# Kernel optimization log

Measured on AMD Instinct MI355X. Metric: run time of the kernel, lower is better.

The kernel has to match this reference:

```python
import jax, jax.numpy as jnp
import numpy as np

EPS = 1e-5  # BatchNorm1d default eps
HEADS = 4


def _batchnorm(x, gamma, beta):
    # BatchNorm1d applied per graph: stats over node axis (axis=1), biased var (training mode)
    mean = x.mean(axis=1, keepdims=True)
    var = x.var(axis=1, keepdims=True)
    return gamma * (x - mean) * jax.lax.rsqrt(var + EPS) + beta


def setup_inputs() -> dict:
    key = jax.random.key(0)
    ks = jax.random.split(key, 8)
    B, N, F_in, C = 4, 4096, 128, 64
    inputs = jax.random.normal(ks[0], (B, N, F_in), jnp.float32)
    # sparse-ish adjacency (avg degree ~16); only used for non-emptiness check since conv=None
    adj = (jax.random.uniform(ks[1], (B, N, N)) < 0.004).astype(jnp.float32)
    s = lambda k, shp, fan: jax.random.normal(k, shp, jnp.float32) / np.sqrt(fan)
    return dict(
        inputs=inputs, adj=adj,
        Wp=s(ks[2], (C, F_in), F_in), bp=jnp.zeros((C,), jnp.float32),      # project Linear
        Wqkv=s(ks[3], (3 * C, C), C), bqkv=jnp.zeros((3 * C,), jnp.float32),  # MHA in_proj
        Wo=s(ks[4], (C, C), C), bo=jnp.zeros((C,), jnp.float32),            # MHA out_proj
        g2=jnp.ones((C,), jnp.float32), b2=jnp.zeros((C,), jnp.float32),    # norm2 (BatchNorm)
        W1=s(ks[5], (2 * C, C), C), b1=jnp.zeros((2 * C,), jnp.float32),    # MLP Linear 1
        W2=s(ks[6], (C, 2 * C), 2 * C), b2m=jnp.zeros((C,), jnp.float32),   # MLP Linear 2
        g3=jnp.ones((C,), jnp.float32), b3=jnp.zeros((C,), jnp.float32),    # norm3 (BatchNorm)
    )


def reference(inputs, adj, Wp, bp, Wqkv, bqkv, Wo, bo, g2, b2, W1, b1, W2, b2m, g3, b3):
    B, N, _ = inputs.shape
    C = Wp.shape[0]
    Dh = C // HEADS
    # project in_features -> out_features
    x = jnp.einsum('bnf,cf->bnc', inputs, Wp) + bp
    # GPSConv with conv=None: only the global multi-head self-attention branch runs
    qkv = jnp.einsum('bnc,dc->bnd', x, Wqkv) + bqkv
    q, k, v = jnp.split(qkv, 3, axis=-1)
    rs = lambda t: t.reshape(B, N, HEADS, Dh)
    q, k, v = rs(q), rs(k), rs(v)
    scores = jnp.einsum('bnhd,bmhd->bhnm', q, k) / np.sqrt(Dh).astype(np.float32)
    attn = jax.nn.softmax(scores, axis=-1)
    o = jnp.einsum('bhnm,bmhd->bnhd', attn, v).reshape(B, N, C)
    h = jnp.einsum('bnc,oc->bno', o, Wo) + bo
    # residual + norm2
    h = _batchnorm(h + x, g2, b2)
    # out = h (sum of single-branch hs); out = out + mlp(out); norm3
    mlp = jnp.einsum('bnk,ck->bnc',
                     jax.nn.relu(jnp.einsum('bnc,kc->bnk', h, W1) + b1),
                     W2) + b2m
    out = _batchnorm(h + mlp, g3, b3)
    # wrapper applies tanh (edge_index non-empty)
    return jnp.tanh(out)
```

## Files before the change

kernel.cpp:

```cpp
#include <hip/hip_runtime.h>
#include <hip/hip_bf16.h>

constexpr int NN = 4096;
constexpr int CC = 64;
constexpr int NH = 4;
constexpr int DH = 16;
constexpr int KSPLIT = 4;

typedef _Float16 f16x4 __attribute__((ext_vector_type(4)));
typedef float f32x4 __attribute__((ext_vector_type(4)));

#define QSCALE 0.36067376022224085f
#define L2E2   2.8853900817779268f

#if defined(__has_builtin)
#if __has_builtin(__builtin_amdgcn_exp2f)
#define FAST_EXP2(x) __builtin_amdgcn_exp2f(x)
#endif
#if __has_builtin(__builtin_amdgcn_rcpf)
#define FAST_RCP(x) __builtin_amdgcn_rcpf(x)
#endif
#endif
#ifndef FAST_EXP2
#define FAST_EXP2(x) exp2f(x)
#endif
#ifndef FAST_RCP
#define FAST_RCP(x) (1.0f / (x))
#endif

__device__ __forceinline__ float fast_tanh(float x) {
  const float t = FAST_EXP2(x * L2E2);
  return fmaf(-2.f, FAST_RCP(t + 1.f), 1.f);
}

__global__ __launch_bounds__(256) void proj_qkv_k(
    const float* __restrict__ inp, const float* __restrict__ Wp,
    const float* __restrict__ bp, const float* __restrict__ Wqkv,
    const float* __restrict__ bqkv, float* __restrict__ xout,
    _Float16* __restrict__ f16b)
{
  __shared__ __align__(16) float As[64][68];
  __shared__ __align__(16) float Xs[64][68];
  __shared__ __align__(16) float W2s[64][196];

  const int tid = threadIdx.x;
  const int rowbase = blockIdx.x * 64;
  const int r4 = (tid & 15) * 4;
  const int cg = (tid >> 4) * 4;
  const int cg2 = (tid >> 4) * 12;

  float acc[4][4];
  #pragma unroll
  for (int i = 0; i < 4; ++i)
    #pragma unroll
    for (int j = 0; j < 4; ++j) acc[i][j] = 0.f;

  for (int k0 = 0; k0 < 128; k0 += 64) {
    if (k0) __syncthreads();
    #pragma unroll
    for (int i = 0; i < 16; ++i) {
      int idx = tid + i * 256;
      int c2 = idx >> 6, kk = idx & 63;
      Xs[kk][c2] = Wp[(size_t)c2 * 128 + k0 + kk];
    }
    #pragma unroll
    for (int i = 0; i < 16; ++i) {
      int idx = tid + i * 256;
      int r = idx >> 6, kk = idx & 63;
      As[kk][r] = inp[(size_t)(rowbase + r) * 128 + k0 + kk];
    }
    __syncthreads();
    #pragma unroll 4
    for (int kk = 0; kk < 64; ++kk) {
      const float4 a = *(const float4*)&As[kk][r4];
      const float4 w4 = *(const float4*)&Xs[kk][cg];
      const float av[4] = {a.x, a.y, a.z, a.w};
      const float wv[4] = {w4.x, w4.y, w4.z, w4.w};
      #pragma unroll
      for (int ri = 0; ri < 4; ++ri)
        #pragma unroll
        for (int ci = 0; ci < 4; ++ci)
          acc[ri][ci] = fmaf(av[ri], wv[ci], acc[ri][ci]);
    }
  }

  float xv[4][4];
  #pragma unroll
  for (int ri = 0; ri < 4; ++ri)
    #pragma unroll
    for (int j = 0; j < 4; ++j) {
      xv[ri][j] = acc[ri][j] + bp[cg + j];
      xout[(size_t)(rowbase + r4 + ri) * CC + cg + j] = xv[ri][j];
    }

  __syncthreads();
  #pragma unroll
  for (int ri = 0; ri < 4; ++ri)
    #pragma unroll
    for (int j = 0; j < 4; ++j)
      Xs[cg + j][r4 + ri] = xv[ri][j];
  #pragma unroll
  for (int i = 0; i < 48; ++i) {
    int idx = tid + i * 256;
    int c2 = idx >> 6, kk = idx & 63;
    W2s[kk][c2] = Wqkv[(size_t)c2 * 64 + kk];
  }
  __syncthreads();

  float acc2[4][12];
  #pragma unroll
  for (int i = 0; i < 4; ++i)
    #pragma unroll
    for (int j = 0; j < 12; ++j) acc2[i][j] = 0.f;

  #pragma unroll 4
  for (int kk = 0; kk < 64; ++kk) {
    const float4 a = *(const float4*)&Xs[kk][r4];
    const float av[4] = {a.x, a.y, a.z, a.w};
    #pragma unroll
    for (int cj = 0; cj < 3; ++cj) {
      const float4 w4 = *(const float4*)&W2s[kk][cg2 + cj * 4];
      const float wv[4] = {w4.x, w4.y, w4.z, w4.w};
      #pragma unroll
      for (int ri = 0; ri < 4; ++ri)
        #pragma unroll
        for (int ci = 0; ci < 4; ++ci)
          acc2[ri][cj * 4 + ci] = fmaf(av[ri], wv[ci], acc2[ri][cj * 4 + ci]);
    }
  }

  #pragma unroll
  for (int ri = 0; ri < 4; ++ri) {
    const int row = rowbase + r4 + ri;
    const int n = row & (NN - 1);
    const int bq = (row >> 12) * NH;
    #pragma unroll
    for (int j = 0; j < 12; ++j) {
      float v = acc2[ri][j] + bqkv[cg2 + j];
      const int c2 = cg2 + j;
      const int which = c2 >> 6;
      const int hc = c2 & 63;
      const int bh = bq + (hc >> 4);
      const int d = hc & 15;
      if (which == 0) v *= QSCALE;
      if (which < 2)
        f16b[(size_t)which * 1048576 + ((size_t)bh * NN + n) * DH + d] = (_Float16)v;
      else
        f16b[2097152 + ((size_t)bh * DH + d) * NN + n] = (_Float16)v;
    }
  }
}

__global__ __launch_bounds__(256, 6) void attn_k(
    const _Float16* __restrict__ qb, const _Float16* __restrict__ kb,
    const _Float16* __restrict__ vtb, float* __restrict__ po,
    float* __restrict__ rs)
{
  __shared__ _Float16 Kl[64][20];
  __shared__ _Float16 Vl[16][72];

  const int bid = blockIdx.x;
  const int xcd = bid & 7;
  const int rest = bid >> 3;
  const int bh = 2 * xcd + (rest & 1);
  const int ks = (rest >> 1) & 3;
  const int n0 = (rest >> 3) * 128;
  const int tid = threadIdx.x;
  const int w = tid >> 6;
  const int l = tid & 63;
  const int g = l >> 4, i = l & 15;
  const int qbase = n0 + w * 32;
  const int kbeg = ks * (NN / KSPLIT);

  const _Float16* __restrict__ qhp = qb + (size_t)bh * NN * DH;
  const _Float16* __restrict__ khp = kb + (size_t)bh * NN * DH;
  const _Float16* __restrict__ vhp = vtb + (size_t)bh * DH * NN;

  const f16x4 qfA = *(const f16x4*)(qhp + (size_t)(qbase + i) * DH + 4 * g);
  const f16x4 qfB = *(const f16x4*)(qhp + (size_t)(qbase + 16 + i) * DH + 4 * g);

  f32x4 oA = {0.f, 0.f, 0.f, 0.f}, oB = {0.f, 0.f, 0.f, 0.f};
  const f32x4 zz = {0.f, 0.f, 0.f, 0.f};
  float rsA = 0.f, rsB = 0.f;

  const int srow = tid >> 2, spart = (tid & 3) * 4;
  const int sd = tid >> 4, scol = (tid & 15) * 4;

  f16x4 kr = *(const f16x4*)(khp + (size_t)(kbeg + srow) * DH + spart);
  f16x4 vr = *(const f16x4*)(vhp + (size_t)sd * NN + kbeg + scol);

  constexpr int NCH = (NN / KSPLIT) / 64;
  for (int c = 0; c < NCH; ++c) {
    *(f16x4*)&Kl[srow][spart] = kr;
    *(f16x4*)&Vl[sd][scol] = vr;
    __syncthreads();
    if (c + 1 < NCH) {
      const int nx = kbeg + (c + 1) * 64;
      kr = *(const f16x4*)(khp + (size_t)(nx + srow) * DH + spart);
      vr = *(const f16x4*)(vhp + (size_t)sd * NN + nx + scol);
    }

    #pragma unroll
    for (int kk = 0; kk < 64; kk += 16) {
      const f16x4 kf = *(const f16x4*)&Kl[kk + i][4 * g];
      const f16x4 vf = *(const f16x4*)&Vl[i][kk + 4 * g];
      f32x4 sA = __builtin_amdgcn_mfma_f32_16x16x16f16(kf, qfA, zz, 0, 0, 0);
      f32x4 sB = __builtin_amdgcn_mfma_f32_16x16x16f16(kf, qfB, zz, 0, 0, 0);
      const float a0 = FAST_EXP2(sA[0]), a1 = FAST_EXP2(sA[1]),
                  a2 = FAST_EXP2(sA[2]), a3 = FAST_EXP2(sA[3]);
      const float b0 = FAST_EXP2(sB[0]), b1 = FAST_EXP2(sB[1]),
                  b2 = FAST_EXP2(sB[2]), b3 = FAST_EXP2(sB[3]);
      rsA += (a0 + a1) + (a2 + a3);
      rsB += (b0 + b1) + (b2 + b3);
      const auto alo = __builtin_amdgcn_cvt_pkrtz(a0, a1);
      const auto ahi = __builtin_amdgcn_cvt_pkrtz(a2, a3);
      const auto blo = __builtin_amdgcn_cvt_pkrtz(b0, b1);
      const auto bhi = __builtin_amdgcn_cvt_pkrtz(b2, b3);
      f16x4 pA, pB;
      pA[0] = (_Float16)alo[0]; pA[1] = (_Float16)alo[1];
      pA[2] = (_Float16)ahi[0]; pA[3] = (_Float16)ahi[1];
      pB[0] = (_Float16)blo[0]; pB[1] = (_Float16)blo[1];
      pB[2] = (_Float16)bhi[0]; pB[3] = (_Float16)bhi[1];
      oA = __builtin_amdgcn_mfma_f32_16x16x16f16(pA, vf, oA, 0, 0, 0);
      oB = __builtin_amdgcn_mfma_f32_16x16x16f16(pB, vf, oB, 0, 0, 0);
    }
    __syncthreads();
  }

  rsA += __shfl_xor(rsA, 16); rsA += __shfl_xor(rsA, 32);
  rsB += __shfl_xor(rsB, 16); rsB += __shfl_xor(rsB, 32);

  float* __restrict__ pob = po + (size_t)(ks * 16 + bh) * NN * DH;
  #pragma unroll
  for (int r = 0; r < 4; ++r) {
    const int ql = 4 * g + r;
    pob[(size_t)(qbase + ql) * DH + i] = oA[r];
    pob[(size_t)(qbase + 16 + ql) * DH + i] = oB[r];
  }
  if (g == 0) {
    float* __restrict__ rsb = rs + (size_t)(ks * 16 + bh) * NN;
    rsb[qbase + i] = rsA;
    rsb[qbase + 16 + i] = rsB;
  }
}

__global__ __launch_bounds__(256) void wo_red_k(
    const float* __restrict__ po, const float* __restrict__ rs,
    const float* __restrict__ Wo, const float* __restrict__ bo,
    const float* __restrict__ xin, float* __restrict__ out)
{
  __shared__ __align__(16) float As[64][68];
  __shared__ __align__(16) float Ws[64][68];
  __shared__ float Linv[64][4];

  const int tid = threadIdx.x;
  const int rowbase = blockIdx.x * 64;
  const int r4 = (tid & 15) * 4;
  const int cg = (tid >> 4) * 4;

  {
    const int r = tid & 63, hb = tid >> 6;
    const int row = rowbase + r;
    const int bh = (row >> 12) * NH + hb;
    const int n = row & (NN - 1);
    const float s = rs[(size_t)bh * NN + n] + rs[(size_t)(16 + bh) * NN + n] +
                    rs[(size_t)(32 + bh) * NN + n] + rs[(size_t)(48 + bh) * NN + n];
    Linv[r][hb] = 1.f / s;
  }
  #pragma unroll
  for (int i = 0; i < 16; ++i) {
    int idx = tid + i * 256;
    int c2 = idx >> 6, kk = idx & 63;
    Ws[kk][c2] = Wo[(size_t)c2 * 64 + kk];
  }
  __syncthreads();
  #pragma unroll
  for (int i = 0; i < 16; ++i) {
    int idx = tid + i * 256;
    int r = idx >> 6, kk = idx & 63;
    const int row = rowbase + r;
    const int bh = (row >> 12) * NH + (kk >> 4);
    const int n = row & (NN - 1);
    const int d = kk & 15;
    const size_t base = (((size_t)bh * NN + n) * DH) + d;
    const float v = po[base] + po[base + 1048576] +
                    po[base + 2097152] + po[base + 3145728];
    As[kk][r] = v * Linv[r][kk >> 4];
  }
  __syncthreads();

  float acc[4][4];
  #pragma unroll
  for (int i = 0; i < 4; ++i)
    #pragma unroll
    for (int j = 0; j < 4; ++j) acc[i][j] = 0.f;

  #pragma unroll 4
  for (int kk = 0; kk < 64; ++kk) {
    const float4 a = *(const float4*)&As[kk][r4];
    const float4 w4 = *(const float4*)&Ws[kk][cg];
    const float av[4] = {a.x, a.y, a.z, a.w};
    const float wv[4] = {w4.x, w4.y, w4.z, w4.w};
    #pragma unroll
    for (int ri = 0; ri < 4; ++ri)
      #pragma unroll
      for (int ci = 0; ci < 4; ++ci)
        acc[ri][ci] = fmaf(av[ri], wv[ci], acc[ri][ci]);
  }

  #pragma unroll
  for (int ri = 0; ri < 4; ++ri) {
    const int row = rowbase + r4 + ri;
    #pragma unroll
    for (int j = 0; j < 4; ++j) {
      const int c = cg + j;
      out[(size_t)row * CC + c] =
          acc[ri][j] + bo[c] + xin[(size_t)row * CC + c];
    }
  }
}

__global__ __launch_bounds__(256) void mlp_k(
    const float* __restrict__ hf, const float* __restrict__ W1,
    const float* __restrict__ b1, const float* __restrict__ W2,
    const float* __restrict__ b2m, float* __restrict__ out)
{
  __shared__ __align__(16) float As[64][68];
  __shared__ __align__(16) float Wbuf[8704];
  __shared__ __align__(16) float Ts[128][68];

  const int tid = threadIdx.x;
  const int rowbase = blockIdx.x * 64;
  const int r4 = (tid & 15) * 4;
  const int cg8 = (tid >> 4) * 8;
  const int cg4 = (tid >> 4) * 4;

  #pragma unroll
  for (int i = 0; i < 32; ++i) {
    int idx = tid + i * 256;
    int c2 = idx >> 6, kk = idx & 63;
    Wbuf[kk * 132 + c2] = W1[(size_t)c2 * 64 + kk];
  }
  #pragma unroll
  for (int i = 0; i < 16; ++i) {
    int idx = tid + i * 256;
    int r = idx >> 6, kk = idx & 63;
    As[kk][r] = hf[(size_t)(rowbase + r) * CC + kk];
  }
  __syncthreads();

  float acc1[4][8];
  #pragma unroll
  for (int i = 0; i < 4; ++i)
    #pragma unroll
    for (int j = 0; j < 8; ++j) acc1[i][j] = 0.f;

  #pragma unroll 4
  for (int kk = 0; kk < 64; ++kk) {
    const float4 a = *(const float4*)&As[kk][r4];
    const float av[4] = {a.x, a.y, a.z, a.w};
    #pragma unroll
    for (int cj = 0; cj < 2; ++cj) {
      const float4 w4 = *(const float4*)&Wbuf[kk * 132 + cg8 + cj * 4];
      const float wv[4] = {w4.x, w4.y, w4.z, w4.w};
      #pragma unroll
      for (int ri = 0; ri < 4; ++ri)
        #pragma unroll
        for (int ci = 0; ci < 4; ++ci)
          acc1[ri][cj * 4 + ci] = fmaf(av[ri], wv[ci], acc1[ri][cj * 4 + ci]);
    }
  }
  #pragma unroll
  for (int ri = 0; ri < 4; ++ri)
    #pragma unroll
    for (int j = 0; j < 8; ++j)
      Ts[cg8 + j][r4 + ri] = fmaxf(acc1[ri][j] + b1[cg8 + j], 0.f);
  __syncthreads();

  #pragma unroll
  for (int i = 0; i < 32; ++i) {
    int idx = tid + i * 256;
    int c2 = idx >> 7, kk = idx & 127;
    Wbuf[kk * 68 + c2] = W2[(size_t)c2 * 128 + kk];
  }
  __syncthreads();

  float acc2[4][4];
  #pragma unroll
  for (int i = 0; i < 4; ++i)
    #pragma unroll
    for (int j = 0; j < 4; ++j) acc2[i][j] = 0.f;

  #pragma unroll 4
  for (int kk = 0; kk < 128; ++kk) {
    const float4 a = *(const float4*)&Ts[kk][r4];
    const float4 w4 = *(const float4*)&Wbuf[kk * 68 + cg4];
    const float av[4] = {a.x, a.y, a.z, a.w};
    const float wv[4] = {w4.x, w4.y, w4.z, w4.w};
    #pragma unroll
    for (int ri = 0; ri < 4; ++ri)
      #pragma unroll
      for (int ci = 0; ci < 4; ++ci)
        acc2[ri][ci] = fmaf(av[ri], wv[ci], acc2[ri][ci]);
  }

  #pragma unroll
  for (int ri = 0; ri < 4; ++ri) {
    const int row = rowbase + r4 + ri;
    #pragma unroll
    for (int j = 0; j < 4; ++j) {
      const int c = cg4 + j;
      out[(size_t)row * CC + c] = acc2[ri][j] + b2m[c] + As[c][r4 + ri];
    }
  }
}

__global__ __launch_bounds__(256) void bn4_k(
    const float* __restrict__ in, const float* __restrict__ g,
    const float* __restrict__ b, float* __restrict__ out, int do_tanh)
{
  const int bb = blockIdx.x >> 4;
  const int c4 = (blockIdx.x & 15) * 4;
  const float* __restrict__ base = in + (size_t)bb * NN * CC + c4;
  const int tid = threadIdx.x;

  float4 s = {0, 0, 0, 0}, sq = {0, 0, 0, 0};
  #pragma unroll
  for (int i = 0; i < 16; ++i) {
    const float4 v = *(const float4*)&base[(size_t)(tid + i * 256) * CC];
    s.x += v.x; s.y += v.y; s.z += v.z; s.w += v.w;
    sq.x = fmaf(v.x, v.x, sq.x); sq.y = fmaf(v.y, v.y, sq.y);
    sq.z = fmaf(v.z, v.z, sq.z); sq.w = fmaf(v.w, v.w, sq.w);
  }
  #pragma unroll
  for (int off = 32; off; off >>= 1) {
    s.x += __shfl_down(s.x, off); s.y += __shfl_down(s.y, off);
    s.z += __shfl_down(s.z, off); s.w += __shfl_down(s.w, off);
    sq.x += __shfl_down(sq.x, off); sq.y += __shfl_down(sq.y, off);
    sq.z += __shfl_down(sq.z, off); sq.w += __shfl_down(sq.w, off);
  }
  __shared__ float red[4][8];
  const int wv = tid >> 6;
  if ((tid & 63) == 0) {
    red[wv][0] = s.x; red[wv][1] = s.y; red[wv][2] = s.z; red[wv][3] = s.w;
    red[wv][4] = sq.x; red[wv][5] = sq.y; red[wv][6] = sq.z; red[wv][7] = sq.w;
  }
  __syncthreads();
  float scale[4], shift[4];
  #pragma unroll
  for (int j = 0; j < 4; ++j) {
    const float ts = red[0][j] + red[1][j] + red[2][j] + red[3][j];
    const float tq = red[0][4 + j] + red[1][4 + j] + red[2][4 + j] + red[3][4 + j];
    const float mean = ts * (1.f / NN);
    const float var = tq * (1.f / NN) - mean * mean;
    const float rstd = rsqrtf(var + 1e-5f);
    scale[j] = g[c4 + j] * rstd;
    shift[j] = b[c4 + j] - mean * scale[j];
  }
  float* __restrict__ ob = out + (size_t)bb * NN * CC + c4;
  #pragma unroll
  for (int i = 0; i < 16; ++i) {
    const size_t idx = (size_t)(tid + i * 256) * CC;
    const float4 v = *(const float4*)&base[idx];
    float4 o;
    o.x = v.x * scale[0] + shift[0];
    o.y = v.y * scale[1] + shift[1];
    o.z = v.z * scale[2] + shift[2];
    o.w = v.w * scale[3] + shift[3];
    if (do_tanh) {
      o.x = fast_tanh(o.x); o.y = fast_tanh(o.y);
      o.z = fast_tanh(o.z); o.w = fast_tanh(o.w);
    }
    *(float4*)&ob[idx] = o;
  }
}

extern "C" void kernel_launch(void* const* d_in, const int* in_sizes, int n_in,
                              void* d_out, int out_size, void* d_ws, size_t ws_size,
                              hipStream_t stream)
{
  const float* inp  = (const float*)d_in[0];
  const float* Wp   = (const float*)d_in[2];
  const float* bp   = (const float*)d_in[3];
  const float* Wqkv = (const float*)d_in[4];
  const float* bqkv = (const float*)d_in[5];
  const float* Wo   = (const float*)d_in[6];
  const float* bo   = (const float*)d_in[7];
  const float* g2   = (const float*)d_in[8];
  const float* b2   = (const float*)d_in[9];
  const float* W1   = (const float*)d_in[10];
  const float* b1   = (const float*)d_in[11];
  const float* W2   = (const float*)d_in[12];
  const float* b2m  = (const float*)d_in[13];
  const float* g3   = (const float*)d_in[14];
  const float* b3   = (const float*)d_in[15];

  float* w = (float*)d_ws;
  float* x    = w;
  float* qkvA = w + 1048576;
  float* hf   = w + 2621440;
  float* pf   = w + 3670016;
  float* poW  = w + 4718592;
  float* rsW  = w + 8912896;

  _Float16* f16b = (_Float16*)qkvA;

  proj_qkv_k<<<dim3(256), dim3(256), 0, stream>>>(inp, Wp, bp, Wqkv, bqkv, x, f16b);
  attn_k<<<dim3(2048), dim3(256), 0, stream>>>(f16b, f16b + 1048576,
                                               f16b + 2097152, poW, rsW);
  wo_red_k<<<dim3(256), dim3(256), 0, stream>>>(poW, rsW, Wo, bo, x, hf);
  bn4_k<<<dim3(64), dim3(256), 0, stream>>>(hf, g2, b2, hf, 0);
  mlp_k<<<dim3(256), dim3(256), 0, stream>>>(hf, W1, b1, W2, b2m, pf);
  bn4_k<<<dim3(64), dim3(256), 0, stream>>>(pf, g3, b3, (float*)d_out, 1);
}
```

Baseline: 125.7 us.

## Split fused projection+QKV kernel into four templated GEMM launches

Replaces the single fused input-projection and QKV kernel with a generic templated GEMM that runs as four launches: the projection, then separate Q, K and V^T GEMMs reading x back from global memory. This likely aims at lower register and LDS use per launch, and so higher occupancy, than the 48-accumulator fused kernel. In exchange it adds three kernel launches and re-reads x from global memory three times.

```diff
diff --git a/kernel.cpp b/kernel.cpp
--- a/kernel.cpp
+++ b/kernel.cpp
@@ -33,120 +33,89 @@
   return fmaf(-2.f, FAST_RCP(t + 1.f), 1.f);
 }
 
-__global__ __launch_bounds__(256) void proj_qkv_k(
-    const float* __restrict__ inp, const float* __restrict__ Wp,
-    const float* __restrict__ bp, const float* __restrict__ Wqkv,
-    const float* __restrict__ bqkv, float* __restrict__ xout,
-    _Float16* __restrict__ f16b)
-{
+enum { EPI_PLAIN = 0, EPI_Q = 1, EPI_K = 2, EPI_VT = 3 };
+
+template<int K, int NC, int EPI>
+__global__ __launch_bounds__(256) void gemm_k(
+    const float* __restrict__ Ain,
+    const float* __restrict__ W,
+    const float* __restrict__ bias,
+    float* __restrict__ out)
+{
+  constexpr int CPT = NC / 16;
   __shared__ __align__(16) float As[64][68];
-  __shared__ __align__(16) float Xs[64][68];
-  __shared__ __align__(16) float W2s[64][196];
+  __shared__ __align__(16) float Ws[64][NC + 4];
 
   const int tid = threadIdx.x;
   const int rowbase = blockIdx.x * 64;
   const int r4 = (tid & 15) * 4;
-  const int cg = (tid >> 4) * 4;
-  const int cg2 = (tid >> 4) * 12;
-
-  float acc[4][4];
+  const int cg = (tid >> 4) * CPT;
+
+  float acc[4][CPT];
   #pragma unroll
   for (int i = 0; i < 4; ++i)
     #pragma unroll
-    for (int j = 0; j < 4; ++j) acc[i][j] = 0.f;
-
-  for (int k0 = 0; k0 < 128; k0 += 64) {
+    for (int j = 0; j < CPT; ++j) acc[i][j] = 0.f;
+
+  for (int k0 = 0; k0 < K; k0 += 64) {
     if (k0) __syncthreads();
     #pragma unroll
-    for (int i = 0; i < 16; ++i) {
+    for (int i = 0; i < (NC * 64) / 256; ++i) {
       int idx = tid + i * 256;
       int c2 = idx >> 6, kk = idx & 63;
-      Xs[kk][c2] = Wp[(size_t)c2 * 128 + k0 + kk];
+      Ws[kk][c2] = W[(size_t)c2 * K + k0 + kk];
     }
     #pragma unroll
     for (int i = 0; i < 16; ++i) {
       int idx = tid + i * 256;
       int r = idx >> 6, kk = idx & 63;
-      As[kk][r] = inp[(size_t)(rowbase + r) * 128 + k0 + kk];
+      As[kk][r] = Ain[(size_t)(rowbase + r) * K + k0 + kk];
     }
     __syncthreads();
+
     #pragma unroll 4
     for (int kk = 0; kk < 64; ++kk) {
       const float4 a = *(const float4*)&As[kk][r4];
-      const float4 w4 = *(const float4*)&Xs[kk][cg];
       const float av[4] = {a.x, a.y, a.z, a.w};
-      const float wv[4] = {w4.x, w4.y, w4.z, w4.w};
       #pragma unroll
-      for (int ri = 0; ri < 4; ++ri)
+      for (int cj = 0; cj < CPT / 4; ++cj) {
+        const float4 wv4 = *(const float4*)&Ws[kk][cg + cj * 4];
+        const float wv[4] = {wv4.x, wv4.y, wv4.z, wv4.w};
         #pragma unroll
-        for (int ci = 0; ci < 4; ++ci)
-          acc[ri][ci] = fmaf(av[ri], wv[ci], acc[ri][ci]);
-    }
-  }
-
-  float xv[4][4];
-  #pragma unroll
-  for (int ri = 0; ri < 4; ++ri)
-    #pragma unroll
-    for (int j = 0; j < 4; ++j) {
-      xv[ri][j] = acc[ri][j] + bp[cg + j];
-      xout[(size_t)(rowbase + r4 + ri) * CC + cg + j] = xv[ri][j];
-    }
-
-  __syncthreads();
-  #pragma unroll
-  for (int ri = 0; ri < 4; ++ri)
-    #pragma unroll
-    for (int j = 0; j < 4; ++j)
-      Xs[cg + j][r4 + ri] = xv[ri][j];
-  #pragma unroll
-  for (int i = 0; i < 48; ++i) {
-    int idx = tid + i * 256;
-    int c2 = idx >> 6, kk = idx & 63;
-    W2s[kk][c2] = Wqkv[(size_t)c2 * 64 + kk];
-  }
-  __syncthreads();
-
-  float acc2[4][12];
-  #pragma unroll
-  for (int i = 0; i < 4; ++i)
-    #pragma unroll
-    for (int j = 0; j < 12; ++j) acc2[i][j] = 0.f;
-
-  #pragma unroll 4
-  for (int kk = 0; kk < 64; ++kk) {
-    const float4 a = *(const float4*)&Xs[kk][r4];
-    const float av[4] = {a.x, a.y, a.z, a.w};
-    #pragma unroll
-    for (int cj = 0; cj < 3; ++cj) {
-      const float4 w4 = *(const float4*)&W2s[kk][cg2 + cj * 4];
-      const float wv[4] = {w4.x, w4.y, w4.z, w4.w};
-      #pragma unroll
-      for (int ri = 0; ri < 4; ++ri)
-        #pragma unroll
-        for (int ci = 0; ci < 4; ++ci)
-          acc2[ri][cj * 4 + ci] = fmaf(av[ri], wv[ci], acc2[ri][cj * 4 + ci]);
-    }
-  }
-
+        for (int ri = 0; ri < 4; ++ri)
+          #pragma unroll
+          for (int ci = 0; ci < 4; ++ci)
+            acc[ri][cj * 4 + ci] = fmaf(av[ri], wv[ci], acc[ri][cj * 4 + ci]);
+      }
+    }
+  }
+
+  float bi[CPT];
+  #pragma unroll
+  for (int j = 0; j < CPT; ++j) bi[j] = bias[cg + j];
+
+  _Float16* f16o = (_Float16*)out;
   #pragma unroll
   for (int ri = 0; ri < 4; ++ri) {
     const int row = rowbase + r4 + ri;
     const int n = row & (NN - 1);
     const int bq = (row >> 12) * NH;
     #pragma unroll
-    for (int j = 0; j < 12; ++j) {
-      float v = acc2[ri][j] + bqkv[cg2 + j];
-      const int c2 = cg2 + j;
-      const int which = c2 >> 6;
-      const int hc = c2 & 63;
-      const int bh = bq + (hc >> 4);
-      const int d = hc & 15;
-      if (which == 0) v *= QSCALE;
-      if (which < 2)
-        f16b[(size_t)which * 1048576 + ((size_t)bh * NN + n) * DH + d] = (_Float16)v;
-      else
-        f16b[2097152 + ((size_t)bh * DH + d) * NN + n] = (_Float16)v;
+    for (int j = 0; j < CPT; ++j) {
+      float v = acc[ri][j] + bi[j];
+      const int c2 = cg + j;
+      if constexpr (EPI == EPI_PLAIN) {
+        out[(size_t)row * NC + c2] = v;
+      } else {
+        const int bh = bq + (c2 >> 4);
+        const int d = c2 & 15;
+        if constexpr (EPI == EPI_Q)
+          f16o[((size_t)bh * NN + n) * DH + d] = (_Float16)(v * QSCALE);
+        if constexpr (EPI == EPI_K)
+          f16o[1048576 + ((size_t)bh * NN + n) * DH + d] = (_Float16)v;
+        if constexpr (EPI == EPI_VT)
+          f16o[2097152 + ((size_t)bh * DH + d) * NN + n] = (_Float16)v;
+      }
     }
   }
 }
@@ -505,7 +474,10 @@
 
   _Float16* f16b = (_Float16*)qkvA;
 
-  proj_qkv_k<<<dim3(256), dim3(256), 0, stream>>>(inp, Wp, bp, Wqkv, bqkv, x, f16b);
+  gemm_k<128, 64, EPI_PLAIN><<<dim3(256), dim3(256), 0, stream>>>(inp, Wp, bp, x);
+  gemm_k<64, 64, EPI_Q><<<dim3(256), dim3(256), 0, stream>>>(x, Wqkv, bqkv, qkvA);
+  gemm_k<64, 64, EPI_K><<<dim3(256), dim3(256), 0, stream>>>(x, Wqkv + 64 * 64, bqkv + 64, qkvA);
+  gemm_k<64, 64, EPI_VT><<<dim3(256), dim3(256), 0, stream>>>(x, Wqkv + 128 * 64, bqkv + 128, qkvA);
   attn_k<<<dim3(2048), dim3(256), 0, stream>>>(f16b, f16b + 1048576,
                                                f16b + 2097152, poW, rsW);
   wo_red_k<<<dim3(256), dim3(256), 0, stream>>>(poW, rsW, Wo, bo, x, hf);
```

Result: no change. 125.4 us (-0.2%).

## Fuse BatchNorm statistics into producers, store attention partials in fp16, halve row tiles

Applied to the files above, without the earlier changes.

Attention partial outputs and row sums are now written as fp16, which halves the split-K partial traffic. The Wo and MLP kernels use 32-row tiles with twice as many blocks, and each emits per-block column sums and sums of squares. The first BatchNorm is applied inside the MLP kernel's load, which removes one standalone BN pass. The final BN+tanh kernel reduces the precomputed partial stats instead of rescanning the data. Storing softmax sums and partials in fp16 loses precision and could overflow on large sums.

```diff
diff --git a/kernel.cpp b/kernel.cpp
--- a/kernel.cpp
+++ b/kernel.cpp
@@ -153,8 +153,8 @@
 
 __global__ __launch_bounds__(256, 6) void attn_k(
     const _Float16* __restrict__ qb, const _Float16* __restrict__ kb,
-    const _Float16* __restrict__ vtb, float* __restrict__ po,
-    float* __restrict__ rs)
+    const _Float16* __restrict__ vtb, _Float16* __restrict__ po,
+    _Float16* __restrict__ rs)
 {
   __shared__ _Float16 Kl[64][20];
   __shared__ _Float16 Vl[16][72];
@@ -230,41 +230,43 @@
   rsA += __shfl_xor(rsA, 16); rsA += __shfl_xor(rsA, 32);
   rsB += __shfl_xor(rsB, 16); rsB += __shfl_xor(rsB, 32);
 
-  float* __restrict__ pob = po + (size_t)(ks * 16 + bh) * NN * DH;
+  _Float16* __restrict__ pob = po + (size_t)(ks * 16 + bh) * NN * DH;
   #pragma unroll
   for (int r = 0; r < 4; ++r) {
     const int ql = 4 * g + r;
-    pob[(size_t)(qbase + ql) * DH + i] = oA[r];
-    pob[(size_t)(qbase + 16 + ql) * DH + i] = oB[r];
+    pob[(size_t)(qbase + ql) * DH + i] = (_Float16)oA[r];
+    pob[(size_t)(qbase + 16 + ql) * DH + i] = (_Float16)oB[r];
   }
   if (g == 0) {
-    float* __restrict__ rsb = rs + (size_t)(ks * 16 + bh) * NN;
-    rsb[qbase + i] = rsA;
-    rsb[qbase + 16 + i] = rsB;
+    _Float16* __restrict__ rsb = rs + (size_t)(ks * 16 + bh) * NN;
+    rsb[qbase + i] = (_Float16)rsA;
+    rsb[qbase + 16 + i] = (_Float16)rsB;
   }
 }
 
 __global__ __launch_bounds__(256) void wo_red_k(
-    const float* __restrict__ po, const float* __restrict__ rs,
+    const _Float16* __restrict__ po, const _Float16* __restrict__ rs,
     const float* __restrict__ Wo, const float* __restrict__ bo,
-    const float* __restrict__ xin, float* __restrict__ out)
+    const float* __restrict__ xin, float* __restrict__ out,
+    float* __restrict__ s2sum, float* __restrict__ s2sq)
 {
-  __shared__ __align__(16) float As[64][68];
+  __shared__ __align__(16) float As[64][36];
   __shared__ __align__(16) float Ws[64][68];
-  __shared__ float Linv[64][4];
+  __shared__ float Linv[32][4];
 
   const int tid = threadIdx.x;
-  const int rowbase = blockIdx.x * 64;
-  const int r4 = (tid & 15) * 4;
+  const int rowbase = blockIdx.x * 32;
+  const int r2 = (tid & 15) * 2;
   const int cg = (tid >> 4) * 4;
 
-  {
-    const int r = tid & 63, hb = tid >> 6;
+  if (tid < 128) {
+    const int r = tid & 31, hb = tid >> 5;
     const int row = rowbase + r;
     const int bh = (row >> 12) * NH + hb;
     const int n = row & (NN - 1);
-    const float s = rs[(size_t)bh * NN + n] + rs[(size_t)(16 + bh) * NN + n] +
-                    rs[(size_t)(32 + bh) * NN + n] + rs[(size_t)(48 + bh) * NN + n];
+    const size_t rb = (size_t)bh * NN + n;
+    const float s = (float)rs[rb] + (float)rs[rb + 65536] +
+                    (float)rs[rb + 131072] + (float)rs[rb + 196608];
     Linv[r][hb] = 1.f / s;
   }
   #pragma unroll
@@ -275,7 +277,7 @@
   }
   __syncthreads();
   #pragma unroll
-  for (int i = 0; i < 16; ++i) {
+  for (int i = 0; i < 8; ++i) {
     int idx = tid + i * 256;
     int r = idx >> 6, kk = idx & 63;
     const int row = rowbase + r;
@@ -283,98 +285,142 @@
     const int n = row & (NN - 1);
     const int d = kk & 15;
     const size_t base = (((size_t)bh * NN + n) * DH) + d;
-    const float v = po[base] + po[base + 1048576] +
-                    po[base + 2097152] + po[base + 3145728];
+    const float v = (float)po[base] + (float)po[base + 1048576] +
+                    (float)po[base + 2097152] + (float)po[base + 3145728];
     As[kk][r] = v * Linv[r][kk >> 4];
   }
   __syncthreads();
 
-  float acc[4][4];
-  #pragma unroll
-  for (int i = 0; i < 4; ++i)
+  float acc[2][4];
+  #pragma unroll
+  for (int i = 0; i < 2; ++i)
     #pragma unroll
     for (int j = 0; j < 4; ++j) acc[i][j] = 0.f;
 
   #pragma unroll 4
   for (int kk = 0; kk < 64; ++kk) {
-    const float4 a = *(const float4*)&As[kk][r4];
+    const float2 a = *(const float2*)&As[kk][r2];
     const float4 w4 = *(const float4*)&Ws[kk][cg];
-    const float av[4] = {a.x, a.y, a.z, a.w};
+    const float av[2] = {a.x, a.y};
     const float wv[4] = {w4.x, w4.y, w4.z, w4.w};
     #pragma unroll
-    for (int ri = 0; ri < 4; ++ri)
+    for (int ri = 0; ri < 2; ++ri)
       #pragma unroll
       for (int ci = 0; ci < 4; ++ci)
         acc[ri][ci] = fmaf(av[ri], wv[ci], acc[ri][ci]);
   }
 
-  #pragma unroll
-  for (int ri = 0; ri < 4; ++ri) {
-    const int row = rowbase + r4 + ri;
+  float vv[2][4];
+  #pragma unroll
+  for (int ri = 0; ri < 2; ++ri) {
+    const int row = rowbase + r2 + ri;
     #pragma unroll
     for (int j = 0; j < 4; ++j) {
       const int c = cg + j;
-      out[(size_t)row * CC + c] =
-          acc[ri][j] + bo[c] + xin[(size_t)row * CC + c];
+      vv[ri][j] = acc[ri][j] + bo[c] + xin[(size_t)row * CC + c];
+      out[(size_t)row * CC + c] = vv[ri][j];
+    }
+  }
+  #pragma unroll
+  for (int j = 0; j < 4; ++j) {
+    float sp = vv[0][j] + vv[1][j];
+    float sq = vv[0][j] * vv[0][j] + vv[1][j] * vv[1][j];
+    #pragma unroll
+    for (int off = 8; off; off >>= 1) {
+      sp += __shfl_down(sp, off);
+      sq += __shfl_down(sq, off);
+    }
+    if ((tid & 15) == 0) {
+      s2sum[(size_t)blockIdx.x * CC + cg + j] = sp;
+      s2sq[(size_t)blockIdx.x * CC + cg + j] = sq;
     }
   }
 }
 
 __global__ __launch_bounds__(256) void mlp_k(
-    const float* __restrict__ hf, const float* __restrict__ W1,
+    const float* __restrict__ pre2, const float* __restrict__ s2sum,
+    const float* __restrict__ s2sq, const float* __restrict__ g2,
+    const float* __restrict__ b2, const float* __restrict__ W1,
     const float* __restrict__ b1, const float* __restrict__ W2,
-    const float* __restrict__ b2m, float* __restrict__ out)
+    const float* __restrict__ b2m, float* __restrict__ out,
+    float* __restrict__ s3sum, float* __restrict__ s3sq)
 {
-  __shared__ __align__(16) float As[64][68];
+  __shared__ __align__(16) float As[64][36];
   __shared__ __align__(16) float Wbuf[8704];
-  __shared__ __align__(16) float Ts[128][68];
+  __shared__ __align__(16) float Ts[128][36];
+  __shared__ float redp[4][64], redq[4][64];
+  __shared__ float sc2[64], sh2[64];
 
   const int tid = threadIdx.x;
-  const int rowbase = blockIdx.x * 64;
-  const int r4 = (tid & 15) * 4;
+  const int rowbase = blockIdx.x * 32;
+  const int bb = blockIdx.x >> 7;
+  const int r2 = (tid & 15) * 2;
   const int cg8 = (tid >> 4) * 8;
   const int cg4 = (tid >> 4) * 4;
 
+  {
+    const int c = tid & 63, part = tid >> 6;
+    float sp = 0.f, sq = 0.f;
+    const int b0 = bb * 128 + part * 32;
+    for (int k = 0; k < 32; ++k) {
+      sp += s2sum[(size_t)(b0 + k) * CC + c];
+      sq += s2sq[(size_t)(b0 + k) * CC + c];
+    }
+    redp[part][c] = sp;
+    redq[part][c] = sq;
+  }
+  __syncthreads();
+  if (tid < 64) {
+    const int c = tid;
+    const float ts = redp[0][c] + redp[1][c] + redp[2][c] + redp[3][c];
+    const float tq = redq[0][c] + redq[1][c] + redq[2][c] + redq[3][c];
+    const float mean = ts * (1.f / NN);
+    const float var = tq * (1.f / NN) - mean * mean;
+    const float rstd = rsqrtf(var + 1e-5f);
+    sc2[c] = g2[c] * rstd;
+    sh2[c] = b2[c] - mean * sc2[c];
+  }
   #pragma unroll
   for (int i = 0; i < 32; ++i) {
     int idx = tid + i * 256;
     int c2 = idx >> 6, kk = idx & 63;
     Wbuf[kk * 132 + c2] = W1[(size_t)c2 * 64 + kk];
   }
-  #pragma unroll
-  for (int i = 0; i < 16; ++i) {
+  __syncthreads();
+  #pragma unroll
+  for (int i = 0; i < 8; ++i) {
     int idx = tid + i * 256;
     int r = idx >> 6, kk = idx & 63;
-    As[kk][r] = hf[(size_t)(rowbase + r) * CC + kk];
-  }
-  __syncthreads();
-
-  float acc1[4][8];
-  #pragma unroll
-  for (int i = 0; i < 4; ++i)
+    As[kk][r] = pre2[(size_t)(rowbase + r) * CC + kk] * sc2[kk] + sh2[kk];
+  }
+  __syncthreads();
+
+  float acc1[2][8];
+  #pragma unroll
+  for (int i = 0; i < 2; ++i)
     #pragma unroll
     for (int j = 0; j < 8; ++j) acc1[i][j] = 0.f;
 
   #pragma unroll 4
   for (int kk = 0; kk < 64; ++kk) {
-    const float4 a = *(const float4*)&As[kk][r4];
-    const float av[4] = {a.x, a.y, a.z, a.w};
+    const float2 a = *(const float2*)&As[kk][r2];
+    const float av[2] = {a.x, a.y};
     #pragma unroll
     for (int cj = 0; cj < 2; ++cj) {
       const float4 w4 = *(const float4*)&Wbuf[kk * 132 + cg8 + cj * 4];
       const float wv[4] = {w4.x, w4.y, w4.z, w4.w};
       #pragma unroll
-      for (int ri = 0; ri < 4; ++ri)
+      for (int ri = 0; ri < 2; ++ri)
         #pragma unroll
         for (int ci = 0; ci < 4; ++ci)
           acc1[ri][cj * 4 + ci] = fmaf(av[ri], wv[ci], acc1[ri][cj * 4 + ci]);
     }
   }
   #pragma unroll
-  for (int ri = 0; ri < 4; ++ri)
+  for (int ri = 0; ri < 2; ++ri)
     #pragma unroll
     for (int j = 0; j < 8; ++j)
-      Ts[cg8 + j][r4 + ri] = fmaxf(acc1[ri][j] + b1[cg8 + j], 0.f);
+      Ts[cg8 + j][r2 + ri] = fmaxf(acc1[ri][j] + b1[cg8 + j], 0.f);
   __syncthreads();
 
   #pragma unroll
@@ -385,92 +431,101 @@
   }
   __syncthreads();
 
-  float acc2[4][4];
-  #pragma unroll
-  for (int i = 0; i < 4; ++i)
+  float acc2[2][4];
+  #pragma unroll
+  for (int i = 0; i < 2; ++i)
     #pragma unroll
     for (int j = 0; j < 4; ++j) acc2[i][j] = 0.f;
 
   #pragma unroll 4
   for (int kk = 0; kk < 128; ++kk) {
-    const float4 a = *(const float4*)&Ts[kk][r4];
+    const float2 a = *(const float2*)&Ts[kk][r2];
     const float4 w4 = *(const float4*)&Wbuf[kk * 68 + cg4];
-    const float av[4] = {a.x, a.y, a.z, a.w};
+    const float av[2] = {a.x, a.y};
     const float wv[4] = {w4.x, w4.y, w4.z, w4.w};
     #pragma unroll
-    for (int ri = 0; ri < 4; ++ri)
+    for (int ri = 0; ri < 2; ++ri)
       #pragma unroll
       for (int ci = 0; ci < 4; ++ci)
         acc2[ri][ci] = fmaf(av[ri], wv[ci], acc2[ri][ci]);
   }
 
-  #pragma unroll
-  for (int ri = 0; ri < 4; ++ri) {
-    const int row = rowbase + r4 + ri;
+  float vv[2][4];
+  #pragma unroll
+  for (int ri = 0; ri < 2; ++ri) {
+    const int row = rowbase + r2 + ri;
     #pragma unroll
     for (int j = 0; j < 4; ++j) {
       const int c = cg4 + j;
-      out[(size_t)row * CC + c] = acc2[ri][j] + b2m[c] + As[c][r4 + ri];
-    }
-  }
-}
-
-__global__ __launch_bounds__(256) void bn4_k(
-    const float* __restrict__ in, const float* __restrict__ g,
-    const float* __restrict__ b, float* __restrict__ out, int do_tanh)
+      vv[ri][j] = acc2[ri][j] + b2m[c] + As[c][r2 + ri];
+      out[(size_t)row * CC + c] = vv[ri][j];
+    }
+  }
+  #pragma unroll
+  for (int j = 0; j < 4; ++j) {
+    float sp = vv[0][j] + vv[1][j];
+    float sq = vv[0][j] * vv[0][j] + vv[1][j] * vv[1][j];
+    #pragma unroll
+    for (int off = 8; off; off >>= 1) {
+      sp += __shfl_down(sp, off);
+      sq += __shfl_down(sq, off);
+    }
+    if ((tid & 15) == 0) {
+      s3sum[(size_t)blockIdx.x * CC + cg4 + j] = sp;
+      s3sq[(size_t)blockIdx.x * CC + cg4 + j] = sq;
+    }
+  }
+}
+
+__global__ __launch_bounds__(1024) void bn_tanh_k(
+    const float* __restrict__ in, const float* __restrict__ s3sum,
+    const float* __restrict__ s3sq, const float* __restrict__ g,
+    const float* __restrict__ b, float* __restrict__ out)
 {
   const int bb = blockIdx.x >> 4;
   const int c4 = (blockIdx.x & 15) * 4;
+  const int tid = threadIdx.x;
+
+  __shared__ float tp[8][4], tq[8][4];
+  __shared__ float scl[4], shf[4];
+  if (tid < 32) {
+    const int j = tid & 3, chunk = tid >> 2;
+    float sp = 0.f, sq = 0.f;
+    const int b0 = bb * 128 + chunk * 16;
+    for (int k = 0; k < 16; ++k) {
+      sp += s3sum[(size_t)(b0 + k) * CC + c4 + j];
+      sq += s3sq[(size_t)(b0 + k) * CC + c4 + j];
+    }
+    tp[chunk][j] = sp;
+    tq[chunk][j] = sq;
+  }
+  __syncthreads();
+  if (tid < 4) {
+    const int j = tid;
+    float ts = 0.f, tqv = 0.f;
+    #pragma unroll
+    for (int k = 0; k < 8; ++k) { ts += tp[k][j]; tqv += tq[k][j]; }
+    const float mean = ts * (1.f / NN);
+    const float var = tqv * (1.f / NN) - mean * mean;
+    const float rstd = rsqrtf(var + 1e-5f);
+    scl[j] = g[c4 + j] * rstd;
+    shf[j] = b[c4 + j] - mean * scl[j];
+  }
+  __syncthreads();
+
+  const float s0 = scl[0], s1 = scl[1], s2 = scl[2], s3 = scl[3];
+  const float h0 = shf[0], h1 = shf[1], h2 = shf[2], h3 = shf[3];
   const float* __restrict__ base = in + (size_t)bb * NN * CC + c4;
-  const int tid = threadIdx.x;
-
-  float4 s = {0, 0, 0, 0}, sq = {0, 0, 0, 0};
-  #pragma unroll
-  for (int i = 0; i < 16; ++i) {
-    const float4 v = *(const float4*)&base[(size_t)(tid + i * 256) * CC];
-    s.x += v.x; s.y += v.y; s.z += v.z; s.w += v.w;
-    sq.x = fmaf(v.x, v.x, sq.x); sq.y = fmaf(v.y, v.y, sq.y);
-    sq.z = fmaf(v.z, v.z, sq.z); sq.w = fmaf(v.w, v.w, sq.w);
-  }
-  #pragma unroll
-  for (int off = 32; off; off >>= 1) {
-    s.x += __shfl_down(s.x, off); s.y += __shfl_down(s.y, off);
-    s.z += __shfl_down(s.z, off); s.w += __shfl_down(s.w, off);
-    sq.x += __shfl_down(sq.x, off); sq.y += __shfl_down(sq.y, off);
-    sq.z += __shfl_down(sq.z, off); sq.w += __shfl_down(sq.w, off);
-  }
-  __shared__ float red[4][8];
-  const int wv = tid >> 6;
-  if ((tid & 63) == 0) {
-    red[wv][0] = s.x; red[wv][1] = s.y; red[wv][2] = s.z; red[wv][3] = s.w;
-    red[wv][4] = sq.x; red[wv][5] = sq.y; red[wv][6] = sq.z; red[wv][7] = sq.w;
-  }
-  __syncthreads();
-  float scale[4], shift[4];
-  #pragma unroll
-  for (int j = 0; j < 4; ++j) {
-    const float ts = red[0][j] + red[1][j] + red[2][j] + red[3][j];
-    const float tq = red[0][4 + j] + red[1][4 + j] + red[2][4 + j] + red[3][4 + j];
-    const float mean = ts * (1.f / NN);
-    const float var = tq * (1.f / NN) - mean * mean;
-    const float rstd = rsqrtf(var + 1e-5f);
-    scale[j] = g[c4 + j] * rstd;
-    shift[j] = b[c4 + j] - mean * scale[j];
-  }
   float* __restrict__ ob = out + (size_t)bb * NN * CC + c4;
   #pragma unroll
-  for (int i = 0; i < 16; ++i) {
-    const size_t idx = (size_t)(tid + i * 256) * CC;
+  for (int i = 0; i < 4; ++i) {
+    const size_t idx = (size_t)(tid + i * 1024) * CC;
     const float4 v = *(const float4*)&base[idx];
     float4 o;
-    o.x = v.x * scale[0] + shift[0];
-    o.y = v.y * scale[1] + shift[1];
-    o.z = v.z * scale[2] + shift[2];
-    o.w = v.w * scale[3] + shift[3];
-    if (do_tanh) {
-      o.x = fast_tanh(o.x); o.y = fast_tanh(o.y);
-      o.z = fast_tanh(o.z); o.w = fast_tanh(o.w);
-    }
+    o.x = fast_tanh(v.x * s0 + h0);
+    o.y = fast_tanh(v.y * s1 + h1);
+    o.z = fast_tanh(v.z * s2 + h2);
+    o.w = fast_tanh(v.w * s3 + h3);
     *(float4*)&ob[idx] = o;
   }
 }
@@ -496,20 +551,28 @@
   const float* b3   = (const float*)d_in[15];
 
   float* w = (float*)d_ws;
-  float* x    = w;
-  float* qkvA = w + 1048576;
-  float* hf   = w + 2621440;
-  float* pf   = w + 3670016;
-  float* poW  = w + 4718592;
-  float* rsW  = w + 8912896;
-
-  _Float16* f16b = (_Float16*)qkvA;
+  float* x     = w;
+  float* qkvA  = w + 1048576;
+  float* pre2  = w + 2621440;
+  float* pre3  = w + 3670016;
+  float* poW   = w + 4718592;
+  float* rsW   = w + 6815744;
+  float* s2s   = w + 7000064;
+  float* s2q   = w + 7032832;
+  float* s3s   = w + 7065600;
+  float* s3q   = w + 7098368;
+
+  _Float16* f16b  = (_Float16*)qkvA;
+  _Float16* po16  = (_Float16*)poW;
+  _Float16* rs16  = (_Float16*)rsW;
 
   proj_qkv_k<<<dim3(256), dim3(256), 0, stream>>>(inp, Wp, bp, Wqkv, bqkv, x, f16b);
   attn_k<<<dim3(2048), dim3(256), 0, stream>>>(f16b, f16b + 1048576,
-                                               f16b + 2097152, poW, rsW);
-  wo_red_k<<<dim3(256), dim3(256), 0, stream>>>(poW, rsW, Wo, bo, x, hf);
-  bn4_k<<<dim3(64), dim3(256), 0, stream>>>(hf, g2, b2, hf, 0);
-  mlp_k<<<dim3(256), dim3(256), 0, stream>>>(hf, W1, b1, W2, b2m, pf);
-  bn4_k<<<dim3(64), dim3(256), 0, stream>>>(pf, g3, b3, (float*)d_out, 1);
-}
+                                               f16b + 2097152, po16, rs16);
+  wo_red_k<<<dim3(512), dim3(256), 0, stream>>>(po16, rs16, Wo, bo, x, pre2,
+                                                s2s, s2q);
+  mlp_k<<<dim3(512), dim3(256), 0, stream>>>(pre2, s2s, s2q, g2, b2,
+                                             W1, b1, W2, b2m, pre3, s3s, s3q);
+  bn_tanh_k<<<dim3(64), dim3(1024), 0, stream>>>(pre3, s3s, s3q, g3, b3,
+                                                 (float*)d_out);
+}
```

After: 102.6 us (median of 2 runs). 18.3% less time.
